# Kernel tuning notes

Hardware: AMD Instinct MI355X
Metric: run time of the kernel (lower is better)

The kernel has to match this reference:

```python
import jax, jax.numpy as jnp
import numpy as np

D = 256          # input_dim
H = 4            # num_heads
W = 4            # window_size
NUM_SCALES = 3
FRACTAL = 2
NUM_CLASSES = 7


def _pool(t, ksize):
    # reflect-pad along time by ksize//2 each side, then avg_pool1d(kernel=stride=ksize)
    p = ksize // 2
    t = jnp.pad(t, ((0, 0), (p, p), (0, 0)), mode='reflect')
    B, Tp, F = t.shape
    L = Tp // ksize
    return t[:, :L * ksize].reshape(B, L, ksize, F).mean(axis=2)


def _window_attn(q, k, v):
    # windowed multi-head self-attention with zero-pad to a multiple of W
    B, T, F = q.shape
    pad = (-T) % W
    if pad:
        q = jnp.pad(q, ((0, 0), (0, pad), (0, 0)))
        k = jnp.pad(k, ((0, 0), (0, pad), (0, 0)))
        v = jnp.pad(v, ((0, 0), (0, pad), (0, 0)))
    Tp = T + pad
    nw = Tp // W
    hd = F // H
    scale = 1.0 / np.sqrt(hd).astype(np.float32)
    # [B, nw, W, H, hd] -> [B, nw, H, W, hd]
    qh = q.reshape(B, nw, W, H, hd).transpose(0, 1, 3, 2, 4)
    kh = k.reshape(B, nw, W, H, hd).transpose(0, 1, 3, 2, 4)
    vh = v.reshape(B, nw, W, H, hd).transpose(0, 1, 3, 2, 4)
    attn = jnp.einsum('bnhqd,bnhkd->bnhqk', qh, kh) * scale
    attn = jax.nn.softmax(attn, axis=-1)
    out = jnp.einsum('bnhqk,bnhkd->bnhqd', attn, vh)
    out = out.transpose(0, 1, 3, 2, 4).reshape(B, Tp, F)
    return out[:, :T]


def _upsample_nearest(f, out_len):
    # matches torch F.interpolate(mode='nearest'): src = floor(i * in / out)
    in_len = f.shape[1]
    idx = jnp.minimum((jnp.arange(out_len) * in_len) // out_len, in_len - 1)
    return f[:, idx]


def setup_inputs() -> dict:
    key = jax.random.key(0)
    ks = jax.random.split(key, 14)
    s = 1.0 / np.sqrt(D).astype(np.float32)
    inp = {
        'x': jax.random.normal(ks[0], (32, 4096, D), dtype=jnp.float32),
        'Wq': jax.random.normal(ks[1], (D, D), dtype=jnp.float32) * s,
        'bq': jnp.zeros((D,), jnp.float32),
        'Wk': jax.random.normal(ks[2], (D, D), dtype=jnp.float32) * s,
        'bk': jnp.zeros((D,), jnp.float32),
        'Wv': jax.random.normal(ks[3], (D, D), dtype=jnp.float32) * s,
        'bv': jnp.zeros((D,), jnp.float32),
        'Wp': jax.random.normal(ks[4], (D, D), dtype=jnp.float32) * s,
        'bp': jnp.zeros((D,), jnp.float32),
        'Wc1': jax.random.normal(ks[5], (D, D), dtype=jnp.float32) * s,
        'bc1': jnp.zeros((D,), jnp.float32),
        'Wc2': jax.random.normal(ks[6], (D, NUM_CLASSES), dtype=jnp.float32) * s,
        'bc2': jnp.zeros((NUM_CLASSES,), jnp.float32),
    }
    return inp


def reference(x, Wq, bq, Wk, bk, Wv, bv, Wp, bp, Wc1, bc1, Wc2, bc2):
    B, T, F = x.shape
    q = x @ Wq + bq
    k = x @ Wk + bk
    v = x @ Wv + bv
    # multi-scale temporal operator + per-scale fractal windowed attention
    outs = []
    for s_idx in range(1, NUM_SCALES + 1):
        ksize = FRACTAL ** (s_idx - 1)
        if ksize == 1:
            qs, ks_, vs = q, k, v
        else:
            qs, ks_, vs = _pool(q, ksize), _pool(k, ksize), _pool(v, ksize)
        outs.append(_window_attn(qs, ks_, vs))
    # scale mixer: nearest upsample + exact GELU + sum + proj
    summed = sum(jax.nn.gelu(_upsample_nearest(f, T), approximate=False) for f in outs)
    fused = summed @ Wp + bp
    # classifier (dropout inactive in eval)
    h = fused.mean(axis=1)
    h = jax.nn.relu(h @ Wc1 + bc1)
    logits = h @ Wc2 + bc2
    return logits
```

## Files before the change

### kernel.cpp

```cpp
#include <hip/hip_runtime.h>

#define DD 256
#define TT 4096
#define BB 32

typedef __attribute__((ext_vector_type(8))) short short8;
typedef __attribute__((ext_vector_type(4))) float floatx4;

__device__ __forceinline__ unsigned short f2bf(float f) {
    unsigned u = __builtin_bit_cast(unsigned, f);
    unsigned r = u + 0x7FFFu + ((u >> 16) & 1u);
    return (unsigned short)(r >> 16);
}
__device__ __forceinline__ float bf2f(unsigned short h) {
    return __builtin_bit_cast(float, (unsigned)h << 16);
}
__device__ __forceinline__ float2 unpk(unsigned u) {
    float2 r;
    r.x = __builtin_bit_cast(float, u << 16);
    r.y = __builtin_bit_cast(float, u & 0xFFFF0000u);
    return r;
}

#define GLDS16(g, l)                                                        \
    __builtin_amdgcn_global_load_lds(                                       \
        (const __attribute__((address_space(1))) void*)(g),                 \
        (__attribute__((address_space(3))) void*)(l), 16, 0, 0)

__global__ __launch_bounds__(256)
void prep_x_kernel(const float* __restrict__ X, unsigned short* __restrict__ Xh)
{
    size_t i = ((size_t)blockIdx.x * 256 + threadIdx.x) * 8;
    float4 a = *(const float4*)(X + i);
    float4 b = *(const float4*)(X + i + 4);
    short8 o;
    o[0] = (short)f2bf(a.x); o[1] = (short)f2bf(a.y);
    o[2] = (short)f2bf(a.z); o[3] = (short)f2bf(a.w);
    o[4] = (short)f2bf(b.x); o[5] = (short)f2bf(b.y);
    o[6] = (short)f2bf(b.z); o[7] = (short)f2bf(b.w);
    *(short8*)(Xh + i) = o;
}

__global__ void prep_w_kernel(const float* __restrict__ Wq,
                              const float* __restrict__ Wk,
                              const float* __restrict__ Wv,
                              unsigned short* __restrict__ Wt)
{
    const int z = blockIdx.y;
    const int k = blockIdx.x;
    const int n = threadIdx.x;
    const float* W = (z == 0) ? Wq : (z == 1) ? Wk : Wv;
    float w = W[k * 256 + n];
    unsigned short hi = f2bf(w);
    unsigned short lo = f2bf(w - bf2f(hi));
    size_t base = (size_t)z * 131072;
    Wt[base +         (size_t)n * 256 + k] = hi;
    Wt[base + 65536 + (size_t)n * 256 + k] = lo;
}

__global__ __launch_bounds__(256, 2)
void qkv_mfma_kernel(const unsigned short* __restrict__ Xh,
                     const unsigned short* __restrict__ Wt,
                     const float* __restrict__ bq, const float* __restrict__ bk,
                     const float* __restrict__ bv,
                     unsigned short* __restrict__ Q, unsigned short* __restrict__ Kp,
                     unsigned short* __restrict__ V)
{
    const int z = blockIdx.z;
    const unsigned short* Wz = Wt + (size_t)z * 131072;
    const float* bias = (z == 0) ? bq : (z == 1) ? bk : bv;
    unsigned short* Y = (z == 0) ? Q : (z == 1) ? Kp : V;

    __shared__ __align__(16) unsigned char smem[32768];
    unsigned short* Asm = (unsigned short*)smem;
    unsigned short* Bsm = (unsigned short*)(smem + 8192);

    const int tid = threadIdx.x;
    const int lane = tid & 63, wave = tid >> 6;
    const int wm = wave & 1, wn = wave >> 1;
    const int l15 = lane & 15, lq = lane >> 4;
    const int col0 = blockIdx.x * 128;
    const size_t row0 = (size_t)blockIdx.y * 128;

    floatx4 acc[4][4];
    #pragma unroll
    for (int i = 0; i < 4; ++i)
        #pragma unroll
        for (int j = 0; j < 4; ++j)
            acc[i][j] = (floatx4){0.f, 0.f, 0.f, 0.f};

    for (int k0 = 0; k0 < 256; k0 += 32) {
        __syncthreads();
        #pragma unroll
        for (int it = 0; it < 2; ++it) {
            int flat = it * 256 + tid;
            int m = flat >> 2, ks = (flat & 3) * 8;
            GLDS16(Xh + (row0 + m) * 256 + k0 + ks, Asm + flat * 8);
        }
        #pragma unroll
        for (int half = 0; half < 2; ++half)
            #pragma unroll
            for (int it = 0; it < 2; ++it) {
                int flat = it * 256 + tid;
                int n = flat >> 2, ks = (flat & 3) * 8;
                GLDS16(Wz + half * 65536 + (size_t)(col0 + n) * 256 + k0 + ks,
                       Bsm + half * 4096 + flat * 8);
            }
        __syncthreads();

        short8 a[4];
        #pragma unroll
        for (int mt = 0; mt < 4; ++mt)
            a[mt] = *(const short8*)(Asm + (wm * 64 + mt * 16 + l15) * 32 + lq * 8);
        #pragma unroll
        for (int nt = 0; nt < 4; ++nt) {
            const unsigned short* bp = Bsm + (wn * 64 + nt * 16 + l15) * 32 + lq * 8;
            short8 bh = *(const short8*)bp;
            short8 bl = *(const short8*)(bp + 4096);
            #pragma unroll
            for (int mt = 0; mt < 4; ++mt) {
                acc[mt][nt] = __builtin_amdgcn_mfma_f32_16x16x32_bf16(a[mt], bh, acc[mt][nt], 0, 0, 0);
                acc[mt][nt] = __builtin_amdgcn_mfma_f32_16x16x32_bf16(a[mt], bl, acc[mt][nt], 0, 0, 0);
            }
        }
    }

    __syncthreads();
    unsigned short* Cs = (unsigned short*)(smem + wave * 8192);
    #pragma unroll
    for (int nt = 0; nt < 4; ++nt) {
        float bv_ = bias[col0 + wn * 64 + nt * 16 + l15];
        #pragma unroll
        for (int mt = 0; mt < 4; ++mt)
            #pragma unroll
            for (int r = 0; r < 4; ++r) {
                int row = mt * 16 + lq * 4 + r;
                Cs[row * 64 + nt * 16 + l15] = f2bf(acc[mt][nt][r] + bv_);
            }
    }
    #pragma unroll
    for (int p = 0; p < 8; ++p) {
        int row = p * 8 + (lane >> 3);
        float4 d = *(const float4*)(Cs + row * 64 + (lane & 7) * 8);
        *(float4*)(Y + (row0 + wm * 64 + row) * 256 + col0 + wn * 64 + (lane & 7) * 8) = d;
    }
}

__device__ __forceinline__ float gelu_exact(float x) {
    return 0.5f * x * (1.0f + erff(x * 0.70710678118654752f));
}
__device__ __forceinline__ void addu4(uint4 d, float* f) {
    float2 t;
    t = unpk(d.x); f[0] += t.x; f[1] += t.y;
    t = unpk(d.y); f[2] += t.x; f[3] += t.y;
    t = unpk(d.z); f[4] += t.x; f[5] += t.y;
    t = unpk(d.w); f[6] += t.x; f[7] += t.y;
}

#define SPAN 32
#define NROW 34
#define STR  264

__global__ __launch_bounds__(256, 2)
void attn_fused_kernel(const unsigned short* __restrict__ Q,
                       const unsigned short* __restrict__ K,
                       const unsigned short* __restrict__ V,
                       float* __restrict__ acc)
{
    __shared__ __align__(16) unsigned char smem[3 * NROW * STR * 2];
    unsigned short* qkvs = (unsigned short*)smem;
    float* scratch = (float*)smem;

    const int tid = threadIdx.x;
    const int s = blockIdx.x;
    const int b = blockIdx.y;
    const int r0 = s * SPAN;

    #pragma unroll
    for (int t = 0; t < 3; ++t) {
        const unsigned short* src = ((t == 0) ? Q : (t == 1) ? K : V) + (size_t)b * TT * DD;
        #pragma unroll
        for (int it = 0; it < 5; ++it) {
            int flat = it * 256 + tid;
            if (flat < NROW * 32) {
                int row = flat >> 5, c = flat & 31;
                int g = r0 - 2 + row;
                g = (g < 0) ? 0 : g;
                uint4 d = *(const uint4*)(src + (size_t)g * DD + c * 8);
                *(uint4*)(qkvs + t * (NROW * STR) + row * STR + c * 8) = d;
            }
        }
    }
    __syncthreads();

    const int slot = tid >> 2, lq = tid & 3;
    const int head = slot & 3, u = slot >> 2;
    int ksize, LEN, w; bool active = true;
    if (u < 8)       { ksize = 1; LEN = 4096; w = s * 8 + u; }
    else if (u < 12) { ksize = 2; LEN = 2049; w = s * 4 + (u - 8); }
    else if (u < 14) { ksize = 4; LEN = 1025; w = s * 2 + (u - 12); }
    else if (u == 14){ ksize = 2; LEN = 2049; w = 512; active = (s == 127); }
    else             { ksize = 4; LEN = 1025; w = 256; active = (s == 127); }

    const int f0 = head * 64 + lq * 16;
    float accL[16];
    #pragma unroll
    for (int i = 0; i < 16; ++i) accL[i] = 0.f;

    if (active) {
        int ridx[4][4]; float cw[4]; bool val[4];
        for (int i = 0; i < 4; ++i) {
            int p = w * 4 + i;
            val[i] = (p < LEN);
            int pc = val[i] ? p : 0;
            int r[4] = {0, 0, 0, 0};
            if (ksize == 1) { r[0] = pc; }
            else if (ksize == 2) {
                if (pc == 0)            { r[0] = 0;      r[1] = 1;      }
                else if (pc == LEN - 1) { r[0] = TT - 2; r[1] = TT - 1; }
                else                    { r[0] = 2 * pc - 1; r[1] = 2 * pc; }
            } else {
                if (pc == 0)            { r[0] = 2; r[1] = 1; r[2] = 0; r[3] = 1; }
                else if (pc == LEN - 1) { r[0] = TT - 3; r[1] = TT - 2; r[2] = TT - 2; r[3] = TT - 1; }
                else                    { r[0] = 4*pc - 2; r[1] = 4*pc - 1; r[2] = 4*pc; r[3] = 4*pc + 1; }
            }
            #pragma unroll
            for (int j = 0; j < 4; ++j) ridx[i][j] = r[j] - (r0 - 2);
            float c = 1.f;
            if (ksize != 1)
                c = (float)(((p + 1) * TT + LEN - 1) / LEN - (p * TT + LEN - 1) / LEN);
            cw[i] = val[i] ? c : 0.f;
        }
        const float inv_k = 1.0f / (float)ksize;

        float S[4][4];
        #pragma unroll
        for (int i = 0; i < 4; ++i)
            #pragma unroll
            for (int j = 0; j < 4; ++j) S[i][j] = 0.f;

        for (int half = 0; half < 2; ++half) {
            float qf[4][8], kf[4][8];
            for (int i = 0; i < 4; ++i) {
                #pragma unroll
                for (int e = 0; e < 8; ++e) { qf[i][e] = 0.f; kf[i][e] = 0.f; }
                if (val[i])
                    for (int j = 0; j < ksize; ++j) {
                        int off = ridx[i][j] * STR + f0 + half * 8;
                        addu4(*(const uint4*)(qkvs + off), qf[i]);
                        addu4(*(const uint4*)(qkvs + NROW * STR + off), kf[i]);
                    }
                #pragma unroll
                for (int e = 0; e < 8; ++e) { qf[i][e] *= inv_k; kf[i][e] *= inv_k; }
            }
            #pragma unroll
            for (int i = 0; i < 4; ++i)
                #pragma unroll
                for (int j = 0; j < 4; ++j) {
                    float d = 0.f;
                    #pragma unroll
                    for (int e = 0; e < 8; ++e) d = fmaf(qf[i][e], kf[j][e], d);
                    S[i][j] += d;
                }
        }
        #pragma unroll
        for (int i = 0; i < 4; ++i)
            #pragma unroll
            for (int j = 0; j < 4; ++j) {
                float t = S[i][j];
                t += __shfl_xor(t, 1, 64);
                t += __shfl_xor(t, 2, 64);
                S[i][j] = t * 0.125f;
            }
        float P[4][4];
        #pragma unroll
        for (int i = 0; i < 4; ++i) {
            float m = fmaxf(fmaxf(S[i][0], S[i][1]), fmaxf(S[i][2], S[i][3]));
            float e0 = __expf(S[i][0] - m), e1 = __expf(S[i][1] - m);
            float e2 = __expf(S[i][2] - m), e3 = __expf(S[i][3] - m);
            float inv = 1.0f / (e0 + e1 + e2 + e3);
            P[i][0] = e0 * inv; P[i][1] = e1 * inv; P[i][2] = e2 * inv; P[i][3] = e3 * inv;
        }
        for (int half = 0; half < 2; ++half) {
            float vf[4][8];
            for (int i = 0; i < 4; ++i) {
                #pragma unroll
                for (int e = 0; e < 8; ++e) vf[i][e] = 0.f;
                if (val[i])
                    for (int j = 0; j < ksize; ++j) {
                        int off = ridx[i][j] * STR + f0 + half * 8;
                        addu4(*(const uint4*)(qkvs + 2 * NROW * STR + off), vf[i]);
                    }
                #pragma unroll
                for (int e = 0; e < 8; ++e) vf[i][e] *= inv_k;
            }
            #pragma unroll
            for (int i = 0; i < 4; ++i) {
                if (!val[i]) continue;
                #pragma unroll
                for (int e = 0; e < 8; ++e) {
                    float o = P[i][0]*vf[0][e] + P[i][1]*vf[1][e]
                            + P[i][2]*vf[2][e] + P[i][3]*vf[3][e];
                    accL[half * 8 + e] += cw[i] * gelu_exact(o);
                }
            }
        }
    }

    __syncthreads();
    #pragma unroll
    for (int e = 0; e < 16; e += 4) {
        float4 d = {accL[e], accL[e+1], accL[e+2], accL[e+3]};
        *(float4*)(scratch + u * 256 + f0 + e) = d;
    }
    __syncthreads();
    float sum = 0.f;
    #pragma unroll
    for (int uu = 0; uu < 16; ++uu) sum += scratch[uu * 256 + tid];
    atomicAdd(&acc[b * DD + tid], sum);
}

__global__ __launch_bounds__(256)
void classifier_kernel(const float* __restrict__ acc,
                       const float* __restrict__ Wp,  const float* __restrict__ bp,
                       const float* __restrict__ Wc1, const float* __restrict__ bc1,
                       const float* __restrict__ Wc2, const float* __restrict__ bc2,
                       float* __restrict__ out)
{
    const int b = blockIdx.x;
    const int d = threadIdx.x;
    __shared__ float sm[256], sf[256], sh[256];

    sm[d] = acc[b * 256 + d] * (1.0f / 4096.0f);
    __syncthreads();

    float s = bp[d];
    for (int kk = 0; kk < 256; ++kk) s = fmaf(sm[kk], Wp[kk * 256 + d], s);
    sf[d] = s;
    __syncthreads();

    s = bc1[d];
    for (int kk = 0; kk < 256; ++kk) s = fmaf(sf[kk], Wc1[kk * 256 + d], s);
    sh[d] = fmaxf(s, 0.0f);
    __syncthreads();

    if (d < 7) {
        s = bc2[d];
        for (int kk = 0; kk < 256; ++kk) s = fmaf(sh[kk], Wc2[kk * 7 + d], s);
        out[b * 7 + d] = s;
    }
}

extern "C" void kernel_launch(void* const* d_in, const int* in_sizes, int n_in,
                              void* d_out, int out_size, void* d_ws, size_t ws_size,
                              hipStream_t stream)
{
    const float* x   = (const float*)d_in[0];
    const float* Wq  = (const float*)d_in[1];
    const float* bq  = (const float*)d_in[2];
    const float* Wk  = (const float*)d_in[3];
    const float* bk  = (const float*)d_in[4];
    const float* Wv  = (const float*)d_in[5];
    const float* bv  = (const float*)d_in[6];
    const float* Wp  = (const float*)d_in[7];
    const float* bp  = (const float*)d_in[8];
    const float* Wc1 = (const float*)d_in[9];
    const float* bc1 = (const float*)d_in[10];
    const float* Wc2 = (const float*)d_in[11];
    const float* bc2 = (const float*)d_in[12];
    float* out = (float*)d_out;

    const size_t plane = (size_t)BB * TT * DD;
    unsigned short* Q  = (unsigned short*)d_ws;
    unsigned short* K  = Q + plane;
    unsigned short* V  = K + plane;
    unsigned short* Xh = V + plane;
    unsigned short* Wt = Xh + plane;
    float* acc = (float*)(Wt + 3 * 131072);

    prep_x_kernel<<<dim3(16384), 256, 0, stream>>>(x, Xh);
    prep_w_kernel<<<dim3(256, 3), 256, 0, stream>>>(Wq, Wk, Wv, Wt);
    (void)hipMemsetAsync(acc, 0, BB * DD * sizeof(float), stream);

    qkv_mfma_kernel<<<dim3(2, 1024, 3), 256, 0, stream>>>(
        Xh, Wt, bq, bk, bv, Q, K, V);

    attn_fused_kernel<<<dim3(128, BB), 256, 0, stream>>>(Q, K, V, acc);

    classifier_kernel<<<dim3(BB), 256, 0, stream>>>(acc, Wp, bp, Wc1, bc1, Wc2, bc2, out);
}
```

Before: 531.7 us.

## Drop split-bf16 weights, widen K tile with swizzled LDS, stream V from global

The QKV projection stops using hi/lo split bf16 weights and runs a single bf16 MFMA pass, halving MFMA work and weight traffic at some cost in accuracy. The GEMM K-tile grows to 64 with an XOR-swizzled LDS layout to cut bank conflicts, and occupancy hints are raised. The attention kernel no longer stages V in LDS and reads it from global memory instead, shrinking LDS so more blocks fit per CU. Pooling divisions are folded into the score scale and into the GELU input, and the upsample count weights are replaced with closed-form expressions specialised to T=4096.

Result: slower. 620.5 us (+16.7%).

```diff
diff --git a/kernel.cpp b/kernel.cpp
--- a/kernel.cpp
+++ b/kernel.cpp
@@ -11,9 +11,6 @@
     unsigned u = __builtin_bit_cast(unsigned, f);
     unsigned r = u + 0x7FFFu + ((u >> 16) & 1u);
     return (unsigned short)(r >> 16);
-}
-__device__ __forceinline__ float bf2f(unsigned short h) {
-    return __builtin_bit_cast(float, (unsigned)h << 16);
 }
 __device__ __forceinline__ float2 unpk(unsigned u) {
     float2 r;
@@ -50,15 +47,10 @@
     const int k = blockIdx.x;
     const int n = threadIdx.x;
     const float* W = (z == 0) ? Wq : (z == 1) ? Wk : Wv;
-    float w = W[k * 256 + n];
-    unsigned short hi = f2bf(w);
-    unsigned short lo = f2bf(w - bf2f(hi));
-    size_t base = (size_t)z * 131072;
-    Wt[base +         (size_t)n * 256 + k] = hi;
-    Wt[base + 65536 + (size_t)n * 256 + k] = lo;
-}
-
-__global__ __launch_bounds__(256, 2)
+    Wt[(size_t)z * 65536 + (size_t)n * 256 + k] = f2bf(W[k * 256 + n]);
+}
+
+__global__ __launch_bounds__(256, 3)
 void qkv_mfma_kernel(const unsigned short* __restrict__ Xh,
                      const unsigned short* __restrict__ Wt,
                      const float* __restrict__ bq, const float* __restrict__ bk,
@@ -67,13 +59,13 @@
                      unsigned short* __restrict__ V)
 {
     const int z = blockIdx.z;
-    const unsigned short* Wz = Wt + (size_t)z * 131072;
+    const unsigned short* Wz = Wt + (size_t)z * 65536;
     const float* bias = (z == 0) ? bq : (z == 1) ? bk : bv;
     unsigned short* Y = (z == 0) ? Q : (z == 1) ? Kp : V;
 
     __shared__ __align__(16) unsigned char smem[32768];
     unsigned short* Asm = (unsigned short*)smem;
-    unsigned short* Bsm = (unsigned short*)(smem + 8192);
+    unsigned short* Bsm = (unsigned short*)(smem + 16384);
 
     const int tid = threadIdx.x;
     const int lane = tid & 63, wave = tid >> 6;
@@ -89,40 +81,40 @@
         for (int j = 0; j < 4; ++j)
             acc[i][j] = (floatx4){0.f, 0.f, 0.f, 0.f};
 
-    for (int k0 = 0; k0 < 256; k0 += 32) {
+    for (int k0 = 0; k0 < 256; k0 += 64) {
         __syncthreads();
         #pragma unroll
-        for (int it = 0; it < 2; ++it) {
+        for (int it = 0; it < 4; ++it) {
             int flat = it * 256 + tid;
-            int m = flat >> 2, ks = (flat & 3) * 8;
-            GLDS16(Xh + (row0 + m) * 256 + k0 + ks, Asm + flat * 8);
-        }
-        #pragma unroll
-        for (int half = 0; half < 2; ++half)
-            #pragma unroll
-            for (int it = 0; it < 2; ++it) {
-                int flat = it * 256 + tid;
-                int n = flat >> 2, ks = (flat & 3) * 8;
-                GLDS16(Wz + half * 65536 + (size_t)(col0 + n) * 256 + k0 + ks,
-                       Bsm + half * 4096 + flat * 8);
-            }
+            int m = flat >> 3, c = flat & 7;
+            GLDS16(Xh + (row0 + m) * 256 + k0 + ((c ^ (m & 7)) * 8), Asm + flat * 8);
+        }
+        #pragma unroll
+        for (int it = 0; it < 4; ++it) {
+            int flat = it * 256 + tid;
+            int n = flat >> 3, c = flat & 7;
+            GLDS16(Wz + (size_t)(col0 + n) * 256 + k0 + ((c ^ (n & 7)) * 8), Bsm + flat * 8);
+        }
         __syncthreads();
 
-        short8 a[4];
+        short8 a[4][2];
         #pragma unroll
         for (int mt = 0; mt < 4; ++mt)
-            a[mt] = *(const short8*)(Asm + (wm * 64 + mt * 16 + l15) * 32 + lq * 8);
-        #pragma unroll
-        for (int nt = 0; nt < 4; ++nt) {
-            const unsigned short* bp = Bsm + (wn * 64 + nt * 16 + l15) * 32 + lq * 8;
-            short8 bh = *(const short8*)bp;
-            short8 bl = *(const short8*)(bp + 4096);
-            #pragma unroll
-            for (int mt = 0; mt < 4; ++mt) {
-                acc[mt][nt] = __builtin_amdgcn_mfma_f32_16x16x32_bf16(a[mt], bh, acc[mt][nt], 0, 0, 0);
-                acc[mt][nt] = __builtin_amdgcn_mfma_f32_16x16x32_bf16(a[mt], bl, acc[mt][nt], 0, 0, 0);
-            }
-        }
+            #pragma unroll
+            for (int kk = 0; kk < 2; ++kk) {
+                int row = wm * 64 + mt * 16 + l15;
+                a[mt][kk] = *(const short8*)(Asm + row * 64 + (((kk * 4 + lq) ^ (l15 & 7)) * 8));
+            }
+        #pragma unroll
+        for (int kk = 0; kk < 2; ++kk)
+            #pragma unroll
+            for (int nt = 0; nt < 4; ++nt) {
+                int rn = wn * 64 + nt * 16 + l15;
+                short8 b = *(const short8*)(Bsm + rn * 64 + (((kk * 4 + lq) ^ (l15 & 7)) * 8));
+                #pragma unroll
+                for (int mt = 0; mt < 4; ++mt)
+                    acc[mt][nt] = __builtin_amdgcn_mfma_f32_16x16x32_bf16(a[mt][kk], b, acc[mt][nt], 0, 0, 0);
+            }
     }
 
     __syncthreads();
@@ -160,25 +152,27 @@
 #define SPAN 32
 #define NROW 34
 #define STR  264
-
-__global__ __launch_bounds__(256, 2)
+#define PLQ  (NROW * STR)
+
+__global__ __launch_bounds__(256, 4)
 void attn_fused_kernel(const unsigned short* __restrict__ Q,
                        const unsigned short* __restrict__ K,
                        const unsigned short* __restrict__ V,
                        float* __restrict__ acc)
 {
-    __shared__ __align__(16) unsigned char smem[3 * NROW * STR * 2];
-    unsigned short* qkvs = (unsigned short*)smem;
+    __shared__ __align__(16) unsigned char smem[2 * PLQ * 2];
+    unsigned short* qks = (unsigned short*)smem;
     float* scratch = (float*)smem;
 
     const int tid = threadIdx.x;
     const int s = blockIdx.x;
     const int b = blockIdx.y;
     const int r0 = s * SPAN;
-
-    #pragma unroll
-    for (int t = 0; t < 3; ++t) {
-        const unsigned short* src = ((t == 0) ? Q : (t == 1) ? K : V) + (size_t)b * TT * DD;
+    const unsigned short* vsrc = V + (size_t)b * TT * DD;
+
+    #pragma unroll
+    for (int t = 0; t < 2; ++t) {
+        const unsigned short* src = ((t == 0) ? Q : K) + (size_t)b * TT * DD;
         #pragma unroll
         for (int it = 0; it < 5; ++it) {
             int flat = it * 256 + tid;
@@ -187,7 +181,7 @@
                 int g = r0 - 2 + row;
                 g = (g < 0) ? 0 : g;
                 uint4 d = *(const uint4*)(src + (size_t)g * DD + c * 8);
-                *(uint4*)(qkvs + t * (NROW * STR) + row * STR + c * 8) = d;
+                *(uint4*)(qks + t * PLQ + row * STR + c * 8) = d;
             }
         }
     }
@@ -208,7 +202,9 @@
     for (int i = 0; i < 16; ++i) accL[i] = 0.f;
 
     if (active) {
-        int ridx[4][4]; float cw[4]; bool val[4];
+        int ridx[4][4];
+        int rg[4][4];
+        float cw[4]; bool val[4];
         for (int i = 0; i < 4; ++i) {
             int p = w * 4 + i;
             val[i] = (p < LEN);
@@ -225,13 +221,15 @@
                 else                    { r[0] = 4*pc - 2; r[1] = 4*pc - 1; r[2] = 4*pc; r[3] = 4*pc + 1; }
             }
             #pragma unroll
-            for (int j = 0; j < 4; ++j) ridx[i][j] = r[j] - (r0 - 2);
-            float c = 1.f;
-            if (ksize != 1)
-                c = (float)(((p + 1) * TT + LEN - 1) / LEN - (p * TT + LEN - 1) / LEN);
+            for (int j = 0; j < 4; ++j) { rg[i][j] = r[j]; ridx[i][j] = r[j] - (r0 - 2); }
+            float c;
+            if (ksize == 1)      c = 1.f;
+            else if (ksize == 2) c = (pc == 1024 || pc == 2048) ? 1.f : 2.f;
+            else                 c = ((pc & 255) == 0 && pc != 0) ? 3.f : 4.f;
             cw[i] = val[i] ? c : 0.f;
         }
         const float inv_k = 1.0f / (float)ksize;
+        const float sscale = 0.125f * inv_k * inv_k;
 
         float S[4][4];
         #pragma unroll
@@ -247,11 +245,9 @@
                 if (val[i])
                     for (int j = 0; j < ksize; ++j) {
                         int off = ridx[i][j] * STR + f0 + half * 8;
-                        addu4(*(const uint4*)(qkvs + off), qf[i]);
-                        addu4(*(const uint4*)(qkvs + NROW * STR + off), kf[i]);
+                        addu4(*(const uint4*)(qks + off), qf[i]);
+                        addu4(*(const uint4*)(qks + PLQ + off), kf[i]);
                     }
-                #pragma unroll
-                for (int e = 0; e < 8; ++e) { qf[i][e] *= inv_k; kf[i][e] *= inv_k; }
             }
             #pragma unroll
             for (int i = 0; i < 4; ++i)
@@ -270,7 +266,7 @@
                 float t = S[i][j];
                 t += __shfl_xor(t, 1, 64);
                 t += __shfl_xor(t, 2, 64);
-                S[i][j] = t * 0.125f;
+                S[i][j] = t * sscale;
             }
         float P[4][4];
         #pragma unroll
@@ -287,12 +283,8 @@
                 #pragma unroll
                 for (int e = 0; e < 8; ++e) vf[i][e] = 0.f;
                 if (val[i])
-                    for (int j = 0; j < ksize; ++j) {
-                        int off = ridx[i][j] * STR + f0 + half * 8;
-                        addu4(*(const uint4*)(qkvs + 2 * NROW * STR + off), vf[i]);
-                    }
-                #pragma unroll
-                for (int e = 0; e < 8; ++e) vf[i][e] *= inv_k;
+                    for (int j = 0; j < ksize; ++j)
+                        addu4(*(const uint4*)(vsrc + (size_t)rg[i][j] * DD + f0 + half * 8), vf[i]);
             }
             #pragma unroll
             for (int i = 0; i < 4; ++i) {
@@ -301,7 +293,7 @@
                 for (int e = 0; e < 8; ++e) {
                     float o = P[i][0]*vf[0][e] + P[i][1]*vf[1][e]
                             + P[i][2]*vf[2][e] + P[i][3]*vf[3][e];
-                    accL[half * 8 + e] += cw[i] * gelu_exact(o);
+                    accL[half * 8 + e] += cw[i] * gelu_exact(o * inv_k);
                 }
             }
         }
@@ -376,7 +368,7 @@
     unsigned short* V  = K + plane;
     unsigned short* Xh = V + plane;
     unsigned short* Wt = Xh + plane;
-    float* acc = (float*)(Wt + 3 * 131072);
+    float* acc = (float*)(Wt + 3 * 65536);
 
     prep_x_kernel<<<dim3(16384), 256, 0, stream>>>(x, Xh);
     prep_w_kernel<<<dim3(256, 3), 256, 0, stream>>>(Wq, Wk, Wv, Wt);
```
